# Optimization experiments

Hardware: AMD Instinct MI355X
Metric: run time of the kernel (lower is better)

## Reference

```python
import jax, jax.numpy as jnp
import numpy as np

B, C = 2000000, 24

def setup_inputs() -> dict:
    key = jax.random.key(0)
    k1, k2 = jax.random.split(key)
    input = jax.random.normal(k1, (B, C), dtype=jnp.float32)
    target = jax.random.randint(k2, (B, C), 0, 2, dtype=jnp.int32)
    return {"input": input, "target": target}

def reference(input, target):
    # LSEP: loss = log1p( sum_i sum_{p in pos_i, n in neg_i} exp(x_in - x_ip) ) / B
    # The ragged double loop factorizes per row:
    #   sum_{p,n} exp(x_n - x_p) = (sum_n exp(x_n)) * (sum_p exp(-x_p))
    pos = target > 0
    neg = target == 0
    s_neg = jnp.sum(jnp.where(neg, jnp.exp(input), 0.0), axis=1)   # [B]
    s_pos = jnp.sum(jnp.where(pos, jnp.exp(-input), 0.0), axis=1)  # [B]
    total = jnp.sum(s_neg * s_pos)
    batch_size = input.shape[0]
    return jnp.log1p(total) / batch_size
```

## Files before the change

### kernel.cpp

```cpp
#include <hip/hip_runtime.h>
#include <math.h>


constexpr int ROWS = 2000000;
constexpr int COLS = 24;
constexpr int BLOCK = 256;
constexpr int GRID = 2048;

__global__ void lsep_zero_ws(double* ws) {
    ws[0] = 0.0;
}

__global__ __launch_bounds__(BLOCK) void lsep_main(
        const float* __restrict__ input,
        const int*   __restrict__ target,
        double*      __restrict__ ws) {
    const int tid    = blockIdx.x * blockDim.x + threadIdx.x;
    const int stride = gridDim.x * blockDim.x;

    double acc = 0.0;

    for (int row = tid; row < ROWS; row += stride) {
        const float4* __restrict__ fin = reinterpret_cast<const float4*>(input + (size_t)row * COLS);
        const int4*   __restrict__ tin = reinterpret_cast<const int4*>(target + (size_t)row * COLS);

        float s_neg = 0.0f;
        float s_pos = 0.0f;

        #pragma unroll
        for (int j = 0; j < 6; ++j) {
            const float4 x = fin[j];
            const int4   t = tin[j];
            float e;
            e = __expf(t.x > 0 ? -x.x : x.x); if (t.x > 0) s_pos += e; else s_neg += e;
            e = __expf(t.y > 0 ? -x.y : x.y); if (t.y > 0) s_pos += e; else s_neg += e;
            e = __expf(t.z > 0 ? -x.z : x.z); if (t.z > 0) s_pos += e; else s_neg += e;
            e = __expf(t.w > 0 ? -x.w : x.w); if (t.w > 0) s_pos += e; else s_neg += e;
        }
        acc += (double)s_neg * (double)s_pos;
    }

    #pragma unroll
    for (int off = 32; off > 0; off >>= 1)
        acc += __shfl_down(acc, off, 64);

    __shared__ double sdata[BLOCK / 64];
    const int lane = threadIdx.x & 63;
    const int wave = threadIdx.x >> 6;
    if (lane == 0) sdata[wave] = acc;
    __syncthreads();

    if (threadIdx.x == 0) {
        double s = 0.0;
        #pragma unroll
        for (int w = 0; w < BLOCK / 64; ++w) s += sdata[w];
        atomicAdd(ws, s);
    }
}

__global__ void lsep_finalize(const double* __restrict__ ws, float* __restrict__ out) {
    out[0] = (float)(log1p(ws[0]) / (double)ROWS);
}

extern "C" void kernel_launch(void* const* d_in, const int* in_sizes, int n_in,
                              void* d_out, int out_size, void* d_ws, size_t ws_size,
                              hipStream_t stream) {
    const float* input  = (const float*)d_in[0];
    const int*   target = (const int*)d_in[1];
    float*       out    = (float*)d_out;
    double*      ws     = (double*)d_ws;

    lsep_zero_ws<<<1, 1, 0, stream>>>(ws);
    lsep_main<<<GRID, BLOCK, 0, stream>>>(input, target, ws);
    lsep_finalize<<<1, 1, 0, stream>>>(ws, out);
}
```

Baseline: 375.4 us.

## Coalesce row loads via tiled float4 reads with LDS regrouping; drop atomics

```diff
diff --git a/kernel.cpp b/kernel.cpp
--- a/kernel.cpp
+++ b/kernel.cpp
@@ -2,75 +2,99 @@
 #include <math.h>
 
 
-constexpr int ROWS = 2000000;
-constexpr int COLS = 24;
-constexpr int BLOCK = 256;
-constexpr int GRID = 2048;
-
-__global__ void lsep_zero_ws(double* ws) {
-    ws[0] = 0.0;
-}
+constexpr int  ROWS  = 2000000;
+constexpr int  BLOCK = 256;
+constexpr int  GRID  = 2048;
+constexpr int  TILE  = 256;
+constexpr int  NT    = (ROWS + TILE - 1) / TILE;
+constexpr long TOT4  = (long)ROWS * 6;
 
 __global__ __launch_bounds__(BLOCK) void lsep_main(
-        const float* __restrict__ input,
-        const int*   __restrict__ target,
-        double*      __restrict__ ws) {
-    const int tid    = blockIdx.x * blockDim.x + threadIdx.x;
-    const int stride = gridDim.x * blockDim.x;
+        const float4* __restrict__ input,
+        const int4*   __restrict__ target,
+        double*       __restrict__ partials)
+{
+    __shared__ float  lds_a[TILE * 7];
+    __shared__ float  lds_b[TILE * 7];
+    __shared__ double sred[BLOCK / 64];
 
+    const int t = threadIdx.x;
     double acc = 0.0;
 
-    for (int row = tid; row < ROWS; row += stride) {
-        const float4* __restrict__ fin = reinterpret_cast<const float4*>(input + (size_t)row * COLS);
-        const int4*   __restrict__ tin = reinterpret_cast<const int4*>(target + (size_t)row * COLS);
+    for (int tile = blockIdx.x; tile < NT; tile += GRID) {
+        const long base4 = (long)tile * (TILE * 6);
 
-        float s_neg = 0.0f;
-        float s_pos = 0.0f;
+        float4 x[6]; int4 tg[6]; bool ok[6];
+        #pragma unroll
+        for (int k = 0; k < 6; ++k) {
+            const long g4 = base4 + t + k * BLOCK;
+            ok[k] = (g4 < TOT4);
+            if (ok[k]) { x[k] = input[g4]; tg[k] = target[g4]; }
+        }
 
         #pragma unroll
-        for (int j = 0; j < 6; ++j) {
-            const float4 x = fin[j];
-            const int4   t = tin[j];
-            float e;
-            e = __expf(t.x > 0 ? -x.x : x.x); if (t.x > 0) s_pos += e; else s_neg += e;
-            e = __expf(t.y > 0 ? -x.y : x.y); if (t.y > 0) s_pos += e; else s_neg += e;
-            e = __expf(t.z > 0 ? -x.z : x.z); if (t.z > 0) s_pos += e; else s_neg += e;
-            e = __expf(t.w > 0 ? -x.w : x.w); if (t.w > 0) s_pos += e; else s_neg += e;
+        for (int k = 0; k < 6; ++k) {
+            if (ok[k]) {
+                float a = 0.0f, b = 0.0f, e;
+                e = __expf(tg[k].x > 0 ? -x[k].x : x[k].x); if (tg[k].x > 0) b += e; else a += e;
+                e = __expf(tg[k].y > 0 ? -x[k].y : x[k].y); if (tg[k].y > 0) b += e; else a += e;
+                e = __expf(tg[k].z > 0 ? -x[k].z : x[k].z); if (tg[k].z > 0) b += e; else a += e;
+                e = __expf(tg[k].w > 0 ? -x[k].w : x[k].w); if (tg[k].w > 0) b += e; else a += e;
+                const int lr  = t + k * BLOCK;
+                const int row = lr / 6;
+                const int j   = lr - row * 6;
+                lds_a[row * 7 + j] = a;
+                lds_b[row * 7 + j] = b;
+            }
         }
-        acc += (double)s_neg * (double)s_pos;
+        __syncthreads();
+
+        const long grow = (long)tile * TILE + t;
+        if (grow < ROWS) {
+            const int r7 = t * 7;
+            const float sa = ((lds_a[r7+0] + lds_a[r7+1]) + (lds_a[r7+2] + lds_a[r7+3]))
+                           +  (lds_a[r7+4] + lds_a[r7+5]);
+            const float sb = ((lds_b[r7+0] + lds_b[r7+1]) + (lds_b[r7+2] + lds_b[r7+3]))
+                           +  (lds_b[r7+4] + lds_b[r7+5]);
+            acc += (double)sa * (double)sb;
+        }
+        __syncthreads();
     }
 
     #pragma unroll
     for (int off = 32; off > 0; off >>= 1)
         acc += __shfl_down(acc, off, 64);
-
-    __shared__ double sdata[BLOCK / 64];
-    const int lane = threadIdx.x & 63;
-    const int wave = threadIdx.x >> 6;
-    if (lane == 0) sdata[wave] = acc;
+    if ((t & 63) == 0) sred[t >> 6] = acc;
     __syncthreads();
-
-    if (threadIdx.x == 0) {
-        double s = 0.0;
-        #pragma unroll
-        for (int w = 0; w < BLOCK / 64; ++w) s += sdata[w];
-        atomicAdd(ws, s);
-    }
+    if (t == 0)
+        partials[blockIdx.x] = (sred[0] + sred[1]) + (sred[2] + sred[3]);
 }
 
-__global__ void lsep_finalize(const double* __restrict__ ws, float* __restrict__ out) {
-    out[0] = (float)(log1p(ws[0]) / (double)ROWS);
+__global__ void lsep_finalize(const double* __restrict__ partials,
+                              float* __restrict__ out)
+{
+    __shared__ double sred[4];
+    const int t = threadIdx.x;
+    double s = 0.0;
+    #pragma unroll
+    for (int i = 0; i < GRID / 256; ++i) s += partials[t + i * 256];
+    #pragma unroll
+    for (int off = 32; off > 0; off >>= 1)
+        s += __shfl_down(s, off, 64);
+    if ((t & 63) == 0) sred[t >> 6] = s;
+    __syncthreads();
+    if (t == 0)
+        out[0] = (float)(log1p((sred[0] + sred[1]) + (sred[2] + sred[3])) / (double)ROWS);
 }
 
 extern "C" void kernel_launch(void* const* d_in, const int* in_sizes, int n_in,
                               void* d_out, int out_size, void* d_ws, size_t ws_size,
                               hipStream_t stream) {
-    const float* input  = (const float*)d_in[0];
-    const int*   target = (const int*)d_in[1];
-    float*       out    = (float*)d_out;
-    double*      ws     = (double*)d_ws;
+    const float4* input  = (const float4*)d_in[0];
+    const int4*   target = (const int4*)d_in[1];
+    double*       ws     = (double*)d_ws;
+    float*        out    = (float*)d_out;
 
-    lsep_zero_ws<<<1, 1, 0, stream>>>(ws);
     lsep_main<<<GRID, BLOCK, 0, stream>>>(input, target, ws);
-    lsep_finalize<<<1, 1, 0, stream>>>(ws, out);
+    lsep_finalize<<<1, 256, 0, stream>>>(ws, out);
 }
```

New measurement: 381.1 us. About the same (+1.5%).
